# Optimization experiments

Hardware: AMD Instinct MI355X
Metric: run time of the kernel (lower is better)

Reference implementation:

```python
import jax, jax.numpy as jnp
import numpy as np

IMAGE_SIZE = 256
NEAR = 0.1
FAR = 100.0
EPS = 1e-3
BACKGROUND = (0.0, 0.0, 0.0)
CHUNK = 64   # faces per scan step (bounds peak memory of the z-buffer pass)
TINY = 1e-12


def _bary(vx, vy, vz, xp, yp):
    """Barycentric weights / perspective-correct depth at pixel centers.
    vx, vy, vz: 3-tuples of vertex coords, broadcastable with xp/yp.
    Mirrors the CUDA kernel: unnormalized cross-product weights, normalize,
    clamp to [0,1], renormalize, zp = 1 / sum(w_k / z_k), near/far clip."""
    x0, x1, x2 = vx; y0, y1, y2 = vy; z0, z1, z2 = vz
    w0 = yp * (x2 - x1) + xp * (y1 - y2) + (x1 * y2 - x2 * y1)
    w1 = yp * (x0 - x2) + xp * (y2 - y0) + (x2 * y0 - x0 * y2)
    w2 = yp * (x1 - x0) + xp * (y0 - y1) + (x0 * y1 - x1 * y0)
    det = w0 + w1 + w2
    safe_det = jnp.where(jnp.abs(det) > TINY, det, 1.0)
    n0, n1, n2 = w0 / safe_det, w1 / safe_det, w2 / safe_det
    inside = (n0 > 0) & (n1 > 0) & (n2 > 0) & (jnp.abs(det) > TINY)
    n0 = jnp.clip(n0, 0.0, 1.0); n1 = jnp.clip(n1, 0.0, 1.0); n2 = jnp.clip(n2, 0.0, 1.0)
    s = n0 + n1 + n2
    s = jnp.where(s > TINY, s, 1.0)
    n0, n1, n2 = n0 / s, n1 / s, n2 / s
    inv_zp = n0 / z0 + n1 / z1 + n2 / z2
    inv_zp = jnp.where(jnp.abs(inv_zp) > TINY, inv_zp, 1.0)
    zp = 1.0 / inv_zp
    valid = inside & (zp > NEAR) & (zp < FAR)
    return (n0, n1, n2), zp, valid


def _pixel_coords():
    IS = IMAGE_SIZE
    return (2.0 * jnp.arange(IS, dtype=jnp.float32) + 1.0 - IS) / IS


def _forward(faces, textures):
    B, F = faces.shape[:2]
    IS = IMAGE_SIZE
    ii = _pixel_coords()

    # ---- pass 1: z-buffer (face-index argmin), chunked scan over faces ----
    # index selection is non-differentiable -> stop_gradient keeps vjp cheap
    fsg = jax.lax.stop_gradient(faces)
    n_chunks = F // CHUNK
    fchunks = jnp.transpose(fsg.reshape(B, n_chunks, CHUNK, 3, 3), (1, 0, 2, 3, 4))
    bases = jnp.arange(n_chunks, dtype=jnp.int32) * CHUNK
    xp4 = ii[None, None, None, :]
    yp4 = ii[None, None, :, None]

    def step(carry, inp):
        depth, fidx = carry
        fc, base = inp                               # fc: [B, CHUNK, 3, 3]
        vx = tuple(fc[:, :, k, 0][:, :, None, None] for k in range(3))
        vy = tuple(fc[:, :, k, 1][:, :, None, None] for k in range(3))
        vz = tuple(fc[:, :, k, 2][:, :, None, None] for k in range(3))
        _, zp, valid = _bary(vx, vy, vz, xp4, yp4)   # [B, CHUNK, IS, IS]
        zp = jnp.where(valid, zp, jnp.inf)
        local = jnp.argmin(zp, axis=1).astype(jnp.int32)
        zbest = jnp.min(zp, axis=1)
        better = zbest < depth
        depth = jnp.where(better, zbest, depth)
        fidx = jnp.where(better, base + local, fidx)
        return (depth, fidx), None

    init = (jnp.full((B, IS, IS), FAR, jnp.float32),
            jnp.full((B, IS, IS), -1, jnp.int32))
    (_, fidx), _ = jax.lax.scan(step, init, (fchunks, bases))

    # ---- pass 2: differentiable recompute for winning faces ----
    mask = fidx >= 0
    safe_idx = jnp.maximum(fidx, 0)
    fsel = jnp.take_along_axis(
        faces.reshape(B, F, 9), safe_idx.reshape(B, -1, 1), axis=1
    ).reshape(B, IS, IS, 3, 3)
    vx = tuple(fsel[..., k, 0] for k in range(3))
    vy = tuple(fsel[..., k, 1] for k in range(3))
    vz = tuple(fsel[..., k, 2] for k in range(3))
    w, zp, _ = _bary(vx, vy, vz, ii[None, None, :], ii[None, :, None])
    depth_map = jnp.where(mask, zp, FAR)

    # ---- texture sampling: 8-corner trilinear in the T^3 face texel cube ----
    T = textures.shape[2]
    tif = [jnp.clip(w[k] * (T - 1) * zp / vz[k], 0.0, T - 1 - EPS) for k in range(3)]
    lo = [jnp.floor(t) for t in tif]
    fr = [t - l for t, l in zip(tif, lo)]
    lo = [l.astype(jnp.int32) for l in lo]

    tex_flat = textures.reshape(B, F * T * T * T, 3)
    base_idx = safe_idx * (T * T * T)
    rgb = jnp.zeros((B, IS, IS, 3), faces.dtype)
    for d0 in (0, 1):
        for d1 in (0, 1):
            for d2 in (0, 1):
                wgt = ((fr[0] if d0 else 1.0 - fr[0]) *
                       (fr[1] if d1 else 1.0 - fr[1]) *
                       (fr[2] if d2 else 1.0 - fr[2]))
                idx = base_idx + (lo[0] + d0) * T * T + (lo[1] + d1) * T + (lo[2] + d2)
                smp = jnp.take_along_axis(tex_flat, idx.reshape(B, -1, 1), axis=1)
                rgb = rgb + wgt[..., None] * smp.reshape(B, IS, IS, 3)

    bg = jnp.asarray(BACKGROUND, faces.dtype)
    mf = mask.astype(faces.dtype)[..., None]
    rgb_map = rgb * mf + (1.0 - mf) * bg
    alpha_map = mask.astype(faces.dtype)
    # pack (rgb, alpha, depth) into a single [B, IS, IS, 5] tensor
    return jnp.concatenate([rgb_map, alpha_map[..., None], depth_map[..., None]], axis=-1)


def setup_inputs() -> dict:
    key = jax.random.key(0)
    B, F, T = 4, 4096, 4
    k1, k2, k3, k4, k5 = jax.random.split(key, 5)
    # small triangles scattered over the screen with depths in (near, far)
    ctr = jax.random.uniform(k1, (B, F, 1, 2), minval=-0.95, maxval=0.95)
    off = jax.random.uniform(k2, (B, F, 3, 2), minval=-0.08, maxval=0.08)
    xy = ctr + off
    zc = jax.random.uniform(k3, (B, F, 1, 1), minval=1.0, maxval=50.0)
    zo = jax.random.uniform(k4, (B, F, 3, 1), minval=-0.2, maxval=0.2)
    faces = jnp.concatenate([xy, zc + zo], axis=-1).astype(jnp.float32)
    textures = jax.random.uniform(k5, (B, F, T, T, T, 3), dtype=jnp.float32)
    return {"faces": faces, "textures": textures}


def reference(faces, textures):
    return _forward(faces, textures)
```

## Files before the change

### kernel.cpp

```cpp
#include <hip/hip_runtime.h>

#define IS 256
#define FCOUNT 4096
#define NEARP 0.1f
#define FARP 100.0f
#define TINYF 1e-12f
#define CAP 256
#define GCAP 128
#define DET_GLOBAL 1e-5f

__device__ __forceinline__ float frn(float r) { asm("" : "+v"(r)); return r; }
__device__ __forceinline__ float mulrn(float a, float b) { return frn(a * b); }
__device__ __forceinline__ float addrn(float a, float b) { return frn(a + b); }
__device__ __forceinline__ float subrn(float a, float b) { return frn(a - b); }
__device__ __forceinline__ float divrn(float a, float b) { return frn(a / b); }
__device__ __forceinline__ float fmarn(float a, float b, float c) {
    return frn(__builtin_fmaf(a, b, c));
}

__global__ void zero_counts(int* __restrict__ counts, int* __restrict__ gcount) {
    counts[blockIdx.x * 256 + threadIdx.x] = 0;
    if (threadIdx.x == 0) gcount[blockIdx.x] = 0;
}

__global__ __launch_bounds__(256) void bin_kernel(
    const float* __restrict__ faces, int* __restrict__ counts,
    int* __restrict__ lists, int* __restrict__ gcount,
    int* __restrict__ glist, int B, int F)
{
    const int gid = blockIdx.x * 256 + threadIdx.x;
    if (gid >= B * F) return;
    const int b = gid / F, f = gid - b * F;
    const float* fp = faces + (size_t)gid * 9;
    const float x0 = fp[0], y0 = fp[1];
    const float x1 = fp[3], y1 = fp[4];
    const float x2 = fp[6], y2 = fp[7];
    const float det = (x1 - x0) * (y2 - y0) - (x2 - x0) * (y1 - y0);
    const float ad = fabsf(det);
    if (ad < DET_GLOBAL) {
        const int pos = atomicAdd(&gcount[b], 1);
        if (pos < GCAP) glist[b * GCAP + pos] = f;
        return;
    }
    const float d = 2e-3f + 3e-7f / ad;
    const float lox = fminf(x0, fminf(x1, x2)) - d;
    const float hix = fmaxf(x0, fmaxf(x1, x2)) + d;
    const float loy = fminf(y0, fminf(y1, y2)) - d;
    const float hiy = fmaxf(y0, fmaxf(y1, y2)) + d;
    int tx0 = (int)floorf((256.f * lox + 255.f) * (1.f / 32.f));
    int tx1 = (int)floorf((256.f * hix + 255.f) * (1.f / 32.f));
    int ty0 = (int)floorf((256.f * loy + 255.f) * (1.f / 32.f));
    int ty1 = (int)floorf((256.f * hiy + 255.f) * (1.f / 32.f));
    tx0 = max(tx0, 0); tx1 = min(tx1, 15);
    ty0 = max(ty0, 0); ty1 = min(ty1, 15);
    for (int ty = ty0; ty <= ty1; ++ty)
        for (int tx = tx0; tx <= tx1; ++tx) {
            const int t = (b * 16 + ty) * 16 + tx;
            const int pos = atomicAdd(&counts[t], 1);
            if (pos < CAP) lists[(size_t)t * CAP + pos] = f;
        }
}

__global__ __launch_bounds__(256) void raster_kernel(
    const float* __restrict__ faces,
    const float* __restrict__ textures,
    const int*   __restrict__ counts,
    const int*   __restrict__ lists,
    const int*   __restrict__ gcount,
    const int*   __restrict__ glist,
    float* __restrict__ out,
    int B, int F)
{
    const int tid  = threadIdx.x;
    const int b    = blockIdx.x >> 8;
    const int tile = blockIdx.x & 255;
    const int px   = (tile & 15) * 16 + (tid & 15);
    const int py   = (tile >> 4) * 16 + (tid >> 4);
    const float xp = (float)(2 * px + 1 - IS) * (1.0f / IS);
    const float yp = (float)(2 * py + 1 - IS) * (1.0f / IS);

    __shared__ float4 s_a[256];
    __shared__ float4 s_b[256];
    __shared__ float4 s_c[256];
    __shared__ int    s_idx[256];

    float bestz = FARP;
    int   besti = -1;

    const float* fbase = faces + (size_t)b * F * 9;
    const int cnt  = min(counts[blockIdx.x], CAP);
    const int gcnt = min(gcount[b], GCAP);
    const int total = cnt + gcnt;
    const int* mylist = lists + (size_t)blockIdx.x * CAP;
    const int* gl     = glist + b * GCAP;

    for (int cbase = 0; cbase < total; cbase += 256) {
        const int m = min(total - cbase, 256);
        if (tid < m) {
            const int k = cbase + tid;
            const int f = (k < cnt) ? mylist[k] : gl[k - cnt];
            const float* fp = fbase + (size_t)f * 9;
            const float x0 = fp[0], y0 = fp[1], z0 = fp[2];
            const float x1 = fp[3], y1 = fp[4], z1 = fp[5];
            const float x2 = fp[6], y2 = fp[7], z2 = fp[8];
            const float A0 = subrn(x2, x1), B0 = subrn(y1, y2);
            const float C0 = fmarn(x1, y2, -mulrn(x2, y1));
            const float A1 = subrn(x0, x2), B1 = subrn(y2, y0);
            const float C1 = fmarn(x2, y0, -mulrn(x0, y2));
            const float A2 = subrn(x1, x0), B2 = subrn(y0, y1);
            const float C2 = fmarn(x0, y1, -mulrn(x1, y0));
            s_a[tid] = make_float4(A0, B0, C0, A1);
            s_b[tid] = make_float4(B1, C1, A2, B2);
            s_c[tid] = make_float4(C2, z0, z1, z2);
            s_idx[tid] = f;
        }
        __syncthreads();

        for (int j = 0; j < m; ++j) {
            const float4 fa = s_a[j];
            const float4 fb = s_b[j];
            const float4 fc = s_c[j];
            const float w0 = addrn(fmarn(yp, fa.x, mulrn(xp, fa.y)), fa.z);
            const float w1 = addrn(fmarn(yp, fa.w, mulrn(xp, fb.x)), fb.y);
            const float w2 = addrn(fmarn(yp, fb.z, mulrn(xp, fb.w)), fc.x);
            const float det = addrn(addrn(w0, w1), w2);
            bool ins;
            if (det > TINYF)       ins = (w0 > 0.f) && (w1 > 0.f) && (w2 > 0.f);
            else if (det < -TINYF) ins = (w0 < 0.f) && (w1 < 0.f) && (w2 < 0.f);
            else                   ins = false;
            if (ins) {
                float n0 = divrn(w0, det), n1 = divrn(w1, det), n2 = divrn(w2, det);
                n0 = frn(fminf(fmaxf(n0, 0.f), 1.f));
                n1 = frn(fminf(fmaxf(n1, 0.f), 1.f));
                n2 = frn(fminf(fmaxf(n2, 0.f), 1.f));
                float s = addrn(addrn(n0, n1), n2);
                s = (s > TINYF) ? s : 1.0f;
                n0 = divrn(n0, s); n1 = divrn(n1, s); n2 = divrn(n2, s);
                float iz = addrn(addrn(divrn(n0, fc.y), divrn(n1, fc.z)),
                                 divrn(n2, fc.w));
                iz = (fabsf(iz) > TINYF) ? iz : 1.0f;
                const float zp = divrn(1.0f, iz);
                if (zp > NEARP && zp < FARP) {
                    const int fi = s_idx[j];
                    if (zp < bestz || (zp == bestz && fi < besti)) {
                        bestz = zp;
                        besti = fi;
                    }
                }
            }
        }
        __syncthreads();
    }

    float r = 0.f, g = 0.f, bch = 0.f, alpha = 0.f, depth = FARP;
    if (besti >= 0) {
        const float* fp = fbase + (size_t)besti * 9;
        const float x0 = fp[0], y0 = fp[1], z0 = fp[2];
        const float x1 = fp[3], y1 = fp[4], z1 = fp[5];
        const float x2 = fp[6], y2 = fp[7], z2 = fp[8];
        const float w0 = addrn(fmarn(yp, subrn(x2, x1), mulrn(xp, subrn(y1, y2))),
                               fmarn(x1, y2, -mulrn(x2, y1)));
        const float w1 = addrn(fmarn(yp, subrn(x0, x2), mulrn(xp, subrn(y2, y0))),
                               fmarn(x2, y0, -mulrn(x0, y2)));
        const float w2 = addrn(fmarn(yp, subrn(x1, x0), mulrn(xp, subrn(y0, y1))),
                               fmarn(x0, y1, -mulrn(x1, y0)));
        const float det = addrn(addrn(w0, w1), w2);
        const float sd = (fabsf(det) > TINYF) ? det : 1.0f;
        float n0 = divrn(w0, sd), n1 = divrn(w1, sd), n2 = divrn(w2, sd);
        n0 = frn(fminf(fmaxf(n0, 0.f), 1.f));
        n1 = frn(fminf(fmaxf(n1, 0.f), 1.f));
        n2 = frn(fminf(fmaxf(n2, 0.f), 1.f));
        float s = addrn(addrn(n0, n1), n2);
        s = (s > TINYF) ? s : 1.0f;
        n0 = divrn(n0, s); n1 = divrn(n1, s); n2 = divrn(n2, s);
        float iz = addrn(addrn(divrn(n0, z0), divrn(n1, z1)), divrn(n2, z2));
        iz = (fabsf(iz) > TINYF) ? iz : 1.0f;
        const float zp = divrn(1.0f, iz);
        depth = zp;

        const float t0 = fminf(fmaxf(divrn(mulrn(mulrn(n0, 3.0f), zp), z0), 0.f), 2.999f);
        const float t1 = fminf(fmaxf(divrn(mulrn(mulrn(n1, 3.0f), zp), z1), 0.f), 2.999f);
        const float t2 = fminf(fmaxf(divrn(mulrn(mulrn(n2, 3.0f), zp), z2), 0.f), 2.999f);
        const float l0 = floorf(t0), l1 = floorf(t1), l2 = floorf(t2);
        const float fr0 = subrn(t0, l0), fr1 = subrn(t1, l1), fr2 = subrn(t2, l2);
        const int i0 = (int)l0, i1 = (int)l1, i2 = (int)l2;

        const float* tx = textures + (size_t)(b * F + besti) * 64 * 3;
        for (int d0 = 0; d0 < 2; ++d0)
            for (int d1 = 0; d1 < 2; ++d1)
                for (int d2 = 0; d2 < 2; ++d2) {
                    const float wg = mulrn(mulrn(d0 ? fr0 : subrn(1.0f, fr0),
                                                 d1 ? fr1 : subrn(1.0f, fr1)),
                                           d2 ? fr2 : subrn(1.0f, fr2));
                    const float* tp = tx + ((i0 + d0) * 16 + (i1 + d1) * 4 + (i2 + d2)) * 3;
                    r   = addrn(r,   mulrn(wg, tp[0]));
                    g   = addrn(g,   mulrn(wg, tp[1]));
                    bch = addrn(bch, mulrn(wg, tp[2]));
                }
        alpha = 1.0f;
    }

    float* op = out + (((size_t)b * IS + py) * IS + px) * 5;
    op[0] = r;
    op[1] = g;
    op[2] = bch;
    op[3] = alpha;
    op[4] = depth;
}

extern "C" void kernel_launch(void* const* d_in, const int* in_sizes, int n_in,
                              void* d_out, int out_size, void* d_ws, size_t ws_size,
                              hipStream_t stream) {
    const float* faces    = (const float*)d_in[0];
    const float* textures = (const float*)d_in[1];
    float* out = (float*)d_out;
    const int F = FCOUNT;
    const int B = in_sizes[0] / (F * 9);
    const int ntiles = B * 256;

    int* counts = (int*)d_ws;
    int* gcount = counts + ntiles;
    int* glist  = gcount + B;
    int* lists  = glist + B * GCAP;

    zero_counts<<<dim3(B), dim3(256), 0, stream>>>(counts, gcount);
    bin_kernel<<<dim3((B * F + 255) / 256), dim3(256), 0, stream>>>(
        faces, counts, lists, gcount, glist, B, F);
    raster_kernel<<<dim3(ntiles), dim3(256), 0, stream>>>(
        faces, textures, counts, lists, gcount, glist, out, B, F);
}
```

Baseline: 109.9 us.

## Precompute edge coefficients in bin kernel, read them directly in raster loop

Per-face edge-function coefficients are now computed once in the binning kernel and stored to global float4 arrays. The raster kernel drops its shared-memory staging and barriers and instead reads the coefficients for each listed face with wave-uniform scalar-indexed global loads, relying on cache. The zero-count kernel is also replaced by hipMemsetAsync. This removes redundant coefficient recomputation and block synchronisation. In exchange, every iteration now depends on a global or L2 load latency rather than an LDS read, and the workspace grows.

Measured after the change: 117.1 us. +6.6%, slower.

```diff
diff --git a/kernel.cpp b/kernel.cpp
--- a/kernel.cpp
+++ b/kernel.cpp
@@ -18,23 +18,30 @@
     return frn(__builtin_fmaf(a, b, c));
 }
 
-__global__ void zero_counts(int* __restrict__ counts, int* __restrict__ gcount) {
-    counts[blockIdx.x * 256 + threadIdx.x] = 0;
-    if (threadIdx.x == 0) gcount[blockIdx.x] = 0;
-}
-
 __global__ __launch_bounds__(256) void bin_kernel(
-    const float* __restrict__ faces, int* __restrict__ counts,
-    int* __restrict__ lists, int* __restrict__ gcount,
-    int* __restrict__ glist, int B, int F)
+    const float* __restrict__ faces,
+    float4* __restrict__ cA, float4* __restrict__ cB, float4* __restrict__ cC,
+    int* __restrict__ counts, int* __restrict__ lists,
+    int* __restrict__ gcount, int* __restrict__ glist, int B, int F)
 {
     const int gid = blockIdx.x * 256 + threadIdx.x;
     if (gid >= B * F) return;
-    const int b = gid / F, f = gid - b * F;
+    const int b = gid >> 12, f = gid & (FCOUNT - 1);
     const float* fp = faces + (size_t)gid * 9;
-    const float x0 = fp[0], y0 = fp[1];
-    const float x1 = fp[3], y1 = fp[4];
-    const float x2 = fp[6], y2 = fp[7];
+    const float x0 = fp[0], y0 = fp[1], z0 = fp[2];
+    const float x1 = fp[3], y1 = fp[4], z1 = fp[5];
+    const float x2 = fp[6], y2 = fp[7], z2 = fp[8];
+
+    const float A0 = subrn(x2, x1), B0 = subrn(y1, y2);
+    const float C0 = fmarn(x1, y2, -mulrn(x2, y1));
+    const float A1 = subrn(x0, x2), B1 = subrn(y2, y0);
+    const float C1 = fmarn(x2, y0, -mulrn(x0, y2));
+    const float A2 = subrn(x1, x0), B2 = subrn(y0, y1);
+    const float C2 = fmarn(x0, y1, -mulrn(x1, y0));
+    cA[gid] = make_float4(A0, B0, C0, A1);
+    cB[gid] = make_float4(B1, C1, A2, B2);
+    cC[gid] = make_float4(C2, z0, z1, z2);
+
     const float det = (x1 - x0) * (y2 - y0) - (x2 - x0) * (y1 - y0);
     const float ad = fabsf(det);
     if (ad < DET_GLOBAL) {
@@ -64,12 +71,11 @@
 __global__ __launch_bounds__(256) void raster_kernel(
     const float* __restrict__ faces,
     const float* __restrict__ textures,
-    const int*   __restrict__ counts,
-    const int*   __restrict__ lists,
-    const int*   __restrict__ gcount,
-    const int*   __restrict__ glist,
-    float* __restrict__ out,
-    int B, int F)
+    const float4* __restrict__ cA, const float4* __restrict__ cB,
+    const float4* __restrict__ cC,
+    const int* __restrict__ counts, const int* __restrict__ lists,
+    const int* __restrict__ gcount, const int* __restrict__ glist,
+    float* __restrict__ out, int B, int F)
 {
     const int tid  = threadIdx.x;
     const int b    = blockIdx.x >> 8;
@@ -79,79 +85,52 @@
     const float xp = (float)(2 * px + 1 - IS) * (1.0f / IS);
     const float yp = (float)(2 * py + 1 - IS) * (1.0f / IS);
 
-    __shared__ float4 s_a[256];
-    __shared__ float4 s_b[256];
-    __shared__ float4 s_c[256];
-    __shared__ int    s_idx[256];
-
     float bestz = FARP;
     int   besti = -1;
 
-    const float* fbase = faces + (size_t)b * F * 9;
     const int cnt  = min(counts[blockIdx.x], CAP);
     const int gcnt = min(gcount[b], GCAP);
     const int total = cnt + gcnt;
     const int* mylist = lists + (size_t)blockIdx.x * CAP;
     const int* gl     = glist + b * GCAP;
-
-    for (int cbase = 0; cbase < total; cbase += 256) {
-        const int m = min(total - cbase, 256);
-        if (tid < m) {
-            const int k = cbase + tid;
-            const int f = (k < cnt) ? mylist[k] : gl[k - cnt];
-            const float* fp = fbase + (size_t)f * 9;
-            const float x0 = fp[0], y0 = fp[1], z0 = fp[2];
-            const float x1 = fp[3], y1 = fp[4], z1 = fp[5];
-            const float x2 = fp[6], y2 = fp[7], z2 = fp[8];
-            const float A0 = subrn(x2, x1), B0 = subrn(y1, y2);
-            const float C0 = fmarn(x1, y2, -mulrn(x2, y1));
-            const float A1 = subrn(x0, x2), B1 = subrn(y2, y0);
-            const float C1 = fmarn(x2, y0, -mulrn(x0, y2));
-            const float A2 = subrn(x1, x0), B2 = subrn(y0, y1);
-            const float C2 = fmarn(x0, y1, -mulrn(x1, y0));
-            s_a[tid] = make_float4(A0, B0, C0, A1);
-            s_b[tid] = make_float4(B1, C1, A2, B2);
-            s_c[tid] = make_float4(C2, z0, z1, z2);
-            s_idx[tid] = f;
-        }
-        __syncthreads();
-
-        for (int j = 0; j < m; ++j) {
-            const float4 fa = s_a[j];
-            const float4 fb = s_b[j];
-            const float4 fc = s_c[j];
-            const float w0 = addrn(fmarn(yp, fa.x, mulrn(xp, fa.y)), fa.z);
-            const float w1 = addrn(fmarn(yp, fa.w, mulrn(xp, fb.x)), fb.y);
-            const float w2 = addrn(fmarn(yp, fb.z, mulrn(xp, fb.w)), fc.x);
-            const float det = addrn(addrn(w0, w1), w2);
-            bool ins;
-            if (det > TINYF)       ins = (w0 > 0.f) && (w1 > 0.f) && (w2 > 0.f);
-            else if (det < -TINYF) ins = (w0 < 0.f) && (w1 < 0.f) && (w2 < 0.f);
-            else                   ins = false;
-            if (ins) {
-                float n0 = divrn(w0, det), n1 = divrn(w1, det), n2 = divrn(w2, det);
-                n0 = frn(fminf(fmaxf(n0, 0.f), 1.f));
-                n1 = frn(fminf(fmaxf(n1, 0.f), 1.f));
-                n2 = frn(fminf(fmaxf(n2, 0.f), 1.f));
-                float s = addrn(addrn(n0, n1), n2);
-                s = (s > TINYF) ? s : 1.0f;
-                n0 = divrn(n0, s); n1 = divrn(n1, s); n2 = divrn(n2, s);
-                float iz = addrn(addrn(divrn(n0, fc.y), divrn(n1, fc.z)),
-                                 divrn(n2, fc.w));
-                iz = (fabsf(iz) > TINYF) ? iz : 1.0f;
-                const float zp = divrn(1.0f, iz);
-                if (zp > NEARP && zp < FARP) {
-                    const int fi = s_idx[j];
-                    if (zp < bestz || (zp == bestz && fi < besti)) {
-                        bestz = zp;
-                        besti = fi;
-                    }
+    const int fb = b * F;
+
+    for (int j = 0; j < total; ++j) {
+        const int fid = (j < cnt) ? mylist[j] : gl[j - cnt];
+        const int f = __builtin_amdgcn_readfirstlane(fid);
+        const float4 fa = cA[fb + f];
+        const float4 fb4 = cB[fb + f];
+        const float4 fc = cC[fb + f];
+        const float w0 = addrn(fmarn(yp, fa.x, mulrn(xp, fa.y)), fa.z);
+        const float w1 = addrn(fmarn(yp, fa.w, mulrn(xp, fb4.x)), fb4.y);
+        const float w2 = addrn(fmarn(yp, fb4.z, mulrn(xp, fb4.w)), fc.x);
+        const float det = addrn(addrn(w0, w1), w2);
+        bool ins;
+        if (det > TINYF)       ins = (w0 > 0.f) && (w1 > 0.f) && (w2 > 0.f);
+        else if (det < -TINYF) ins = (w0 < 0.f) && (w1 < 0.f) && (w2 < 0.f);
+        else                   ins = false;
+        if (ins) {
+            float n0 = divrn(w0, det), n1 = divrn(w1, det), n2 = divrn(w2, det);
+            n0 = frn(fminf(fmaxf(n0, 0.f), 1.f));
+            n1 = frn(fminf(fmaxf(n1, 0.f), 1.f));
+            n2 = frn(fminf(fmaxf(n2, 0.f), 1.f));
+            float s = addrn(addrn(n0, n1), n2);
+            s = (s > TINYF) ? s : 1.0f;
+            n0 = divrn(n0, s); n1 = divrn(n1, s); n2 = divrn(n2, s);
+            float iz = addrn(addrn(divrn(n0, fc.y), divrn(n1, fc.z)),
+                             divrn(n2, fc.w));
+            iz = (fabsf(iz) > TINYF) ? iz : 1.0f;
+            const float zp = divrn(1.0f, iz);
+            if (zp > NEARP && zp < FARP) {
+                if (zp < bestz || (zp == bestz && f < besti)) {
+                    bestz = zp;
+                    besti = f;
                 }
             }
         }
-        __syncthreads();
     }
 
+    const float* fbase = faces + (size_t)b * F * 9;
     float r = 0.f, g = 0.f, bch = 0.f, alpha = 0.f, depth = FARP;
     if (besti >= 0) {
         const float* fp = fbase + (size_t)besti * 9;
@@ -222,10 +201,13 @@
     int* gcount = counts + ntiles;
     int* glist  = gcount + B;
     int* lists  = glist + B * GCAP;
-
-    zero_counts<<<dim3(B), dim3(256), 0, stream>>>(counts, gcount);
+    float4* cA  = (float4*)(lists + (size_t)ntiles * CAP);
+    float4* cB  = cA + (size_t)B * F;
+    float4* cC  = cB + (size_t)B * F;
+
+    hipMemsetAsync(counts, 0, (size_t)(ntiles + B) * sizeof(int), stream);
     bin_kernel<<<dim3((B * F + 255) / 256), dim3(256), 0, stream>>>(
-        faces, counts, lists, gcount, glist, B, F);
+        faces, cA, cB, cC, counts, lists, gcount, glist, B, F);
     raster_kernel<<<dim3(ntiles), dim3(256), 0, stream>>>(
-        faces, textures, counts, lists, gcount, glist, out, B, F);
-}
+        faces, textures, cA, cB, cC, counts, lists, gcount, glist, out, B, F);
+}
```
